# Kernel optimization log

Hardware: AMD Instinct MI355X
Metric: run time of the kernel (lower is better)

## Reference

```python
import jax, jax.numpy as jnp
from jax import lax
import numpy as np
from itertools import permutations, combinations

GRID = (8, 8, 8)  # width, height, depth


def _build_complex(size):
    """Freudenthal (Kuhn) triangulation of the 3D voxel grid.

    Equivalent role to scipy Delaunay on the regular grid (which is degenerate
    anyway): 6 tetrahedra per unit cube, plus all unique faces, edges, verts.
    Returns:
      simp_verts [n,4] int32 : vertex ids of each simplex, padded by repetition
      simp_dim   [n]   int32 : simplex dimension 0..3
      bnd_cof, bnd_face [m] int32 : (cofacet_id, face_id) boundary incidences
    """
    W, H, D = size

    def vid(p):
        return (p[..., 0] * H + p[..., 1]) * D + p[..., 2]

    e = np.eye(3, dtype=np.int64)
    gx, gy, gz = np.meshgrid(np.arange(W - 1), np.arange(H - 1), np.arange(D - 1), indexing="ij")
    base = np.stack([gx, gy, gz], -1).reshape(-1, 3)
    tet_list = []
    for p in permutations(range(3)):
        v0 = base
        v1 = v0 + e[p[0]]
        v2 = v1 + e[p[1]]
        v3 = v2 + e[p[2]]
        tet_list.append(np.stack([vid(v0), vid(v1), vid(v2), vid(v3)], -1))
    tets = np.unique(np.sort(np.concatenate(tet_list, 0), axis=1), axis=0)
    c3 = np.array(list(combinations(range(4), 3)))
    tris = np.unique(tets[:, c3].reshape(-1, 3), axis=0)
    c2 = np.array(list(combinations(range(3), 2)))
    edges = np.unique(tris[:, c2].reshape(-1, 2), axis=0)

    nV = W * H * D
    nE, nT = len(edges), len(tris)
    eid = {tuple(ed): nV + i for i, ed in enumerate(edges)}
    tid = {tuple(tr): nV + nE + i for i, tr in enumerate(tris)}

    bc, bf = [], []
    for i, ed in enumerate(edges):
        j = nV + i
        bc += [j, j]
        bf += [int(ed[0]), int(ed[1])]
    for i, tr in enumerate(tris):
        j = nV + nE + i
        for pair in combinations(tr, 2):
            bc.append(j)
            bf.append(eid[pair])
    for i, te in enumerate(tets):
        j = nV + nE + nT + i
        for tri in combinations(te, 3):
            bc.append(j)
            bf.append(tid[tri])

    vpad = np.repeat(np.arange(nV)[:, None], 4, axis=1)
    epad = np.pad(edges, ((0, 0), (0, 2)), mode="edge")
    tpad = np.pad(tris, ((0, 0), (0, 1)), mode="edge")
    simp_verts = np.concatenate([vpad, epad, tpad, tets], 0).astype(np.int32)
    simp_dim = np.concatenate([
        np.zeros(nV), np.ones(nE), 2 * np.ones(nT), 3 * np.ones(len(tets))
    ]).astype(np.int32)
    return simp_verts, simp_dim, np.asarray(bc, np.int32), np.asarray(bf, np.int32)


def setup_inputs() -> dict:
    key = jax.random.key(0)
    sv, sd, bc, bf = _build_complex(GRID)
    beta = jax.random.normal(key, (GRID[0] * GRID[1] * GRID[2],), dtype=jnp.float32)
    return {
        "beta": beta,
        "simp_verts": jnp.asarray(sv),
        "simp_dim": jnp.asarray(sd),
        "bnd_cof": jnp.asarray(bc),
        "bnd_face": jnp.asarray(bf),
    }


def _toploss(beta, simp_verts, simp_dim, bnd_cof, bnd_face):
    n = simp_dim.shape[0]
    # Superlevel-set (sublevel=False) filtration: simplex value = min over vertices.
    f = jnp.min(beta[simp_verts], axis=1)  # [n]
    # Filtration order: f descending, tie-break dimension ascending.
    perm = jnp.lexsort((simp_dim, lax.stop_gradient(-f)))
    inv = jnp.zeros(n, jnp.int32).at[perm].set(jnp.arange(n, dtype=jnp.int32))
    # Boundary matrix over GF(2), stored row-major: B[j] = boundary of simplex j.
    B = jnp.zeros((n, n), dtype=bool).at[inv[bnd_cof], inv[bnd_face]].set(True)

    idxs = jnp.arange(n, dtype=jnp.int32)
    low = lambda row: jnp.max(jnp.where(row, idxs, -1))

    def body(j, state):
        B, piv = state

        def cond(c):
            return (c[1] >= 0) & (piv[c[1]] >= 0)

        def step(c):
            r = c[0] ^ B[piv[c[1]]]
            return r, low(r)

        row = B[j]
        row, l = lax.while_loop(cond, step, (row, low(row)))
        B = B.at[j].set(row)
        piv2 = piv.at[jnp.maximum(l, 0)].set(jnp.asarray(j, jnp.int32))
        piv = jnp.where(l >= 0, piv2, piv)
        return B, piv

    _, piv = lax.fori_loop(0, n, body, (B, jnp.full((n,), -1, jnp.int32)))
    piv = lax.stop_gradient(piv)  # combinatorial pairing: constant wrt beta

    fs = f[perm]           # filtration values in sorted order (differentiable)
    ds = simp_dim[perm]
    paired = piv >= 0      # simplex i born, killed by simplex piv[i]
    lengths = jnp.where(paired, fs - fs[jnp.maximum(piv, 0)], 0.0)  # birth - death >= 0
    # SumBarcodeLengths(dim=0): all finite dim-0 bars (essential bars have length 0).
    loss0 = jnp.sum(jnp.where(ds == 0, lengths, 0.0))
    # PartialSumBarcodeLengths(dim=1, skip=1): sum of dim-1 lengths minus the largest.
    len1 = jnp.where(ds == 1, lengths, 0.0)
    loss1 = jnp.sum(len1) - jnp.max(len1)
    return loss0 + loss1


_toploss_jit = jax.jit(_toploss)


def reference(beta, simp_verts, simp_dim, bnd_cof, bnd_face):
    return _toploss_jit(beta, simp_verts, simp_dim, bnd_cof, bnd_face)
```

## Files before the change

### kernel.cpp

```cpp
#include <hip/hip_runtime.h>
#include <stdint.h>

#define MAX_E 3072
#define MAX_T 4608
#define MAX_V 1024
#define TW    72
#define INF_I 0x7fffffff
#define RB_E  12
#define RB_T  18
#define RB_C  24
#define TBLK  18
#define EP_BITS  14
#define EP_MASK  0x3FFF
#define EP_DONE  0x3FFF

typedef unsigned long long ull;

__device__ int   g_erank[MAX_E];
__device__ int   g_eorder[MAX_E];
__device__ float g_ef[MAX_E];
__device__ int   g_trank[MAX_T];
__device__ float g_tf[MAX_T];
__device__ __attribute__((aligned(16))) ull g_rows[(size_t)MAX_E * TW];
__device__ int   g_mst[MAX_E];
__device__ int   g_clr[MAX_E];
__device__ int   g_ilow[MAX_E];
__device__ float g_loss0;

__device__ __forceinline__ int ub_dim(const int* __restrict__ sd, int nS, int d) {
  int lo = 0, hi = nS;
  while (lo < hi) { int mid = (lo + hi) >> 1; if (sd[mid] <= d) lo = mid + 1; else hi = mid; }
  return lo;
}

__device__ __forceinline__ ull rank_key(float f, int j) {
  unsigned bb = __float_as_uint(f);
  unsigned ord = (bb & 0x80000000u) ? ~bb : (bb | 0x80000000u);
  return ((ull)ord << 32) | (ull)(0xffffffffu - (unsigned)j);
}

__device__ __forceinline__ int rank_count64(const ull* __restrict__ sk, int n, ull ki) {
  int r = 0, j = 0;
  for (; j + 8 <= n; j += 8) {
    ulonglong2 a = *(const ulonglong2*)(sk + j);
    ulonglong2 b = *(const ulonglong2*)(sk + j + 2);
    ulonglong2 c = *(const ulonglong2*)(sk + j + 4);
    ulonglong2 d = *(const ulonglong2*)(sk + j + 6);
    r += (int)(a.x > ki) + (int)(a.y > ki) + (int)(b.x > ki) + (int)(b.y > ki)
       + (int)(c.x > ki) + (int)(c.y > ki) + (int)(d.x > ki) + (int)(d.y > ki);
  }
  for (; j < n; ++j) r += (int)(sk[j] > ki);
  return r;
}

__device__ __forceinline__ int uf_find(int* par, int x) {
  for (;;) {
    int p = par[x];
    if (p == x) return x;
    int gp = par[p];
    if (p != gp) par[x] = gp;
    x = gp;
  }
}

union SharedK1 {
  struct { alignas(16) ull sk[MAX_T]; } rank;
  struct {
    int par[MAX_V]; ull cand[MAX_V]; int hookTo[MAX_V];
    int eu[MAX_E], ev2[MAX_E];
    float efv[MAX_E];
    unsigned int ekey[MAX_E];
    unsigned short alive[2][MAX_E];
    unsigned char mstf[MAX_E];
  } uf;
};

__global__ void __launch_bounds__(256) k_main1(const float* __restrict__ beta,
                                               const int* __restrict__ sv,
                                               const int* __restrict__ sd,
                                               int nV, int nS) {
  __shared__ SharedK1 sh;
  __shared__ float aS[4], aM[4], aW[4];
  __shared__ int nNext;
  int b = blockIdx.x, tid = threadIdx.x;
  int nE = ub_dim(sd, nS, 1) - nV;

  if (b < RB_E) {
    int i = b * 256 + tid;
    float fi = 0.f;
    for (int j = tid; j < nE; j += 256) {
      const int* p = &sv[(size_t)(nV + j) * 4];
      float fj = fminf(beta[p[0]], beta[p[1]]);
      if (j == i) fi = fj;
      sh.rank.sk[j] = rank_key(fj, j);
    }
    __syncthreads();
    if (i >= nE) return;
    int r = rank_count64(sh.rank.sk, nE, sh.rank.sk[i]);
    g_erank[i] = r;
    g_eorder[r] = i;
    g_ef[r] = fi;
    return;
  }
  if (b < RB_E + RB_T) {
    int nT = ub_dim(sd, nS, 2) - nV - nE;
    int base = nV + nE;
    int i = (b - RB_E) * 256 + tid;
    float fi = 0.f;
    for (int j = tid; j < nT; j += 256) {
      const int* p = &sv[(size_t)(base + j) * 4];
      float fj = fminf(fminf(beta[p[0]], beta[p[1]]), beta[p[2]]);
      if (j == i) fi = fj;
      sh.rank.sk[j] = rank_key(fj, j);
    }
    __syncthreads();
    if (i >= nT) return;
    int r = rank_count64(sh.rank.sk, nT, sh.rank.sk[i]);
    g_trank[i] = r;
    g_tf[r] = fi;
    return;
  }
  if (b > RB_E + RB_T) {
    size_t i = (size_t)(b - RB_E - RB_T - 1) * 256 + tid;
    size_t stride = (size_t)RB_C * 256;
    for (size_t k = i; k < (size_t)MAX_E * TW; k += stride) g_rows[k] = 0ull;
    for (size_t k = i; k < MAX_E; k += stride) g_ilow[k] = -1;
    return;
  }

  int lane = tid & 63, wave = tid >> 6;
  int* par = sh.uf.par;
  for (int v = tid; v < nV; v += 256) par[v] = v;
  for (int e = tid; e < nE; e += 256) {
    int u = sv[(size_t)(nV + e) * 4];
    int v = sv[(size_t)(nV + e) * 4 + 1];
    sh.uf.eu[e] = u; sh.uf.ev2[e] = v;
    float fe = fminf(beta[u], beta[v]);
    sh.uf.efv[e] = fe;
    unsigned int bb = __float_as_uint(fe);
    sh.uf.ekey[e] = (bb & 0x80000000u) ? ~bb : (bb | 0x80000000u);
    sh.uf.alive[0][e] = (unsigned short)e;
    sh.uf.mstf[e] = 0;
  }
  float s = 0.f, m = -3.0e38f;
  for (int v = tid; v < nV; v += 256) { float fv = beta[v]; s += fv; m = fmaxf(m, fv); }
  float W = 0.f;
  int nAlive = nE, cur = 0;
  __syncthreads();
  for (int phase = 0; phase < 20 && nAlive > 0; ++phase) {
    for (int v = tid; v < nV; v += 256) sh.uf.cand[v] = 0ull;
    if (tid == 0) nNext = 0;
    __syncthreads();
    for (int i0 = 0; i0 < nAlive; i0 += 256) {
      int i = i0 + tid;
      int e = -1;
      bool cross = false;
      int ra = 0, rb = 0;
      if (i < nAlive) {
        e = sh.uf.alive[cur][i];
        ra = uf_find(par, sh.uf.eu[e]);
        rb = uf_find(par, sh.uf.ev2[e]);
        cross = (ra != rb);
      }
      ull mb = __ballot(cross);
      int base = 0;
      if (lane == 0 && mb) base = atomicAdd(&nNext, __popcll(mb));
      base = __shfl(base, 0);
      if (cross) {
        int off = __popcll(mb & ((1ull << lane) - 1ull));
        sh.uf.alive[cur ^ 1][base + off] = (unsigned short)e;
        ull key = ((ull)sh.uf.ekey[e] << 32) | (ull)(0xffffffffu - (unsigned)e);
        atomicMax(&sh.uf.cand[ra], key);
        atomicMax(&sh.uf.cand[rb], key);
      }
    }
    __syncthreads();
    for (int v = tid; v < nV; v += 256) {
      int t = -1;
      ull cv = sh.uf.cand[v];
      if (par[v] == v && cv) {
        int e = (int)(0xffffffffu - (unsigned)(cv & 0xffffffffu));
        int ra = uf_find(par, sh.uf.eu[e]);
        int rb = uf_find(par, sh.uf.ev2[e]);
        int other = (ra == v) ? rb : ra;
        if (sh.uf.cand[other] != cv || v < other) t = other;
      }
      sh.uf.hookTo[v] = t;
    }
    __syncthreads();
    for (int v = tid; v < nV; v += 256) {
      int t = sh.uf.hookTo[v];
      if (t >= 0) {
        par[v] = t;
        int e = (int)(0xffffffffu - (unsigned)(sh.uf.cand[v] & 0xffffffffu));
        W += sh.uf.efv[e];
        sh.uf.mstf[e] = 1;
      }
    }
    __syncthreads();
    for (int it = 0; it < 2; ++it) {
      for (int v = tid; v < nV; v += 256) {
        int p = par[v]; int gp = par[p];
        if (p != gp) par[v] = gp;
      }
      __syncthreads();
    }
    nAlive = nNext;
    cur ^= 1;
    __syncthreads();
  }
  __syncthreads();
  for (int e = tid; e < nE; e += 256) g_mst[e] = sh.uf.mstf[e];
  #pragma unroll
  for (int off = 32; off; off >>= 1) {
    s += __shfl_xor(s, off, 64);
    m = fmaxf(m, __shfl_xor(m, off, 64));
    W += __shfl_xor(W, off, 64);
  }
  if (lane == 0) { aS[wave] = s; aM[wave] = m; aW[wave] = W; }
  __syncthreads();
  if (tid == 0) {
    float S = 0.f, M = -3.0e38f, WW = 0.f;
    for (int i = 0; i < 4; ++i) { S += aS[i]; M = fmaxf(M, aM[i]); WW += aW[i]; }
    g_loss0 = S - M - WW;
  }
}

__global__ void __launch_bounds__(256) k_scat(const int* __restrict__ bf,
                                              const int* __restrict__ sd,
                                              int nV, int nS) {
  int nE = ub_dim(sd, nS, 1) - nV;
  int tid = threadIdx.x;
  if (blockIdx.x == TBLK) {
    for (int r = tid; r < nE; r += 256)
      g_clr[nE - 1 - r] = g_mst[g_eorder[r]];
    return;
  }
  int nT = ub_dim(sd, nS, 2) - nV - nE;
  int t = blockIdx.x * 256 + tid;
  if (t >= nT) return;
  int lpos = nT - 1 - g_trank[t];
  size_t base = (size_t)2 * nE + (size_t)3 * t;
  ull bit = 1ull << (lpos & 63);
  int word = lpos >> 6;
  for (int j = 0; j < 3; ++j) {
    int e = bf[base + j] - nV;
    int rr = nE - 1 - g_erank[e];
    atomicOr(&g_rows[(size_t)rr * TW + word], bit);
    atomicMax(&g_ilow[rr], lpos);
  }
}

__device__ __forceinline__ int row_low(ull x, ull y, int lane) {
  ull msk = __ballot((x | y) != 0ull);
  int hb = y ? (lane * 128 + 127 - __clzll(y)) : (lane * 128 + 63 - __clzll(x | 1ull));
  return msk ? __shfl(hb, 63 - __clzll(msk)) : -1;
}

__global__ void __launch_bounds__(1024) k_reduce(const int* __restrict__ sd,
                                                 int nV, int nS,
                                                 float* __restrict__ out) {
  __shared__ int spiv[MAX_T];
  __shared__ int lowA[MAX_E];
  __shared__ int lists[2][MAX_E];
  __shared__ int tailq[64];
  __shared__ int cnts[2];
  __shared__ int workIdx;
  __shared__ float ssum[16], smax[16];

  int tid = threadIdx.x;
  int lane = tid & 63;
  int wave = tid >> 6;
  int nE = ub_dim(sd, nS, 1) - nV;
  int nT = ub_dim(sd, nS, 2) - nV - nE;

  for (int i = tid; i < nT; i += 1024) spiv[i] = INF_I;
  if (tid == 0) { cnts[0] = 0; cnts[1] = 0; }
  __syncthreads();

  for (int r = tid; r < nE; r += 1024) {
    int l = g_clr[r] ? -1 : g_ilow[r];
    lowA[r] = l;
    if (l >= 0) atomicMin(&spiv[l], (r << EP_BITS) | EP_DONE);
  }
  __syncthreads();
  for (int r = tid; r < nE; r += 1024) {
    int l = lowA[r];
    if (l >= 0 && (spiv[l] >> EP_BITS) != r) { int q = atomicAdd(&cnts[0], 1); lists[0][q] = r; }
  }
  __syncthreads();

  int pass = 0;
  int cnt = cnts[0];
  while (cnt > 0 && pass < 16000) {
    int cur = pass & 1, nxt = cur ^ 1;

    if (cnt <= 8) {
      if (wave == 0) {
        for (int i = lane; i < cnt; i += 64) tailq[i] = lists[cur][i];
        int head = 0, tl = cnt;
        while (head < tl) {
          int r = tailq[head & 63]; head++;
          int l = lowA[r];
          ull wx = 0, wy = 0;
          bool loaded = false;
          for (;;) {
            int p = spiv[l] >> EP_BITS;
            ull px = 0, py = 0;
            if (lane < 36) {
              ulonglong2 v = *(const ulonglong2*)&g_rows[(size_t)p * TW + 2 * lane];
              px = v.x; py = v.y;
            }
            if (!loaded) {
              if (lane < 36) {
                ulonglong2 v = *(const ulonglong2*)&g_rows[(size_t)r * TW + 2 * lane];
                wx = v.x; wy = v.y;
              }
              loaded = true;
            }
            wx ^= px; wy ^= py;
            l = row_low(wx, wy, lane);
            if (l < 0) break;
            int old = 0;
            if (lane == 0) old = atomicMin(&spiv[l], (r << EP_BITS) | EP_DONE);
            old = __shfl(old, 0);
            if (old > ((r << EP_BITS) | EP_DONE)) {
              if (lane < 36) {
                ulonglong2 v; v.x = wx; v.y = wy;
                *(ulonglong2*)&g_rows[(size_t)r * TW + 2 * lane] = v;
              }
              if (lane == 0) lowA[r] = l;
              if (old != INF_I) { if (lane == 0) tailq[tl & 63] = old >> EP_BITS; tl++; }
              break;
            }
          }
        }
      }
      __syncthreads();
      break;
    }

    if (tid == 0) { cnts[nxt] = 0; workIdx = 0; }
    __syncthreads();
    for (;;) {
      int idx = 0;
      if (lane == 0) idx = atomicAdd(&workIdx, 1);
      idx = __shfl(idx, 0);
      if (idx >= cnt) break;
      int r = lists[cur][idx];
      int l = lowA[r];
      ull wx = 0, wy = 0;
      bool loaded = false, modified = false;
      for (;;) {
        int val = spiv[l];
        int p = val >> EP_BITS;
        if ((val & EP_MASK) == pass) {
          if (lane == 0) { int q = atomicAdd(&cnts[nxt], 1); lists[nxt][q] = r; }
          break;
        }
        ull px = 0, py = 0;
        if (lane < 36) {
          ulonglong2 v = *(const ulonglong2*)&g_rows[(size_t)p * TW + 2 * lane];
          px = v.x; py = v.y;
        }
        if (!loaded) {
          if (lane < 36) {
            ulonglong2 v = *(const ulonglong2*)&g_rows[(size_t)r * TW + 2 * lane];
            wx = v.x; wy = v.y;
          }
          loaded = true;
        }
        wx ^= px; wy ^= py;
        modified = true;
        l = row_low(wx, wy, lane);
        if (lane == 0) lowA[r] = l;
        if (l < 0) break;
        int myval = (r << EP_BITS) | pass;
        int old = 0;
        if (lane == 0) old = atomicMin(&spiv[l], myval);
        old = __shfl(old, 0);
        if (old > myval) {
          if (old != INF_I && lane == 0) { int q = atomicAdd(&cnts[nxt], 1); lists[nxt][q] = old >> EP_BITS; }
          break;
        }
      }
      if (modified && l >= 0 && lane < 36) {
        ulonglong2 v; v.x = wx; v.y = wy;
        *(ulonglong2*)&g_rows[(size_t)r * TW + 2 * lane] = v;
      }
    }
    __syncthreads();
    cnt = cnts[nxt];
    pass++;
  }

  float sum = 0.f, mx = 0.f;
  for (int l = tid; l < nT; l += 1024) {
    int v = spiv[l];
    if (v != INF_I) {
      int r = v >> EP_BITS;
      float len = g_ef[nE - 1 - r] - g_tf[nT - 1 - l];
      sum += len;
      mx = fmaxf(mx, len);
    }
  }
  #pragma unroll
  for (int off = 32; off; off >>= 1) {
    sum += __shfl_xor(sum, off, 64);
    mx = fmaxf(mx, __shfl_xor(mx, off, 64));
  }
  if (lane == 0) { ssum[wave] = sum; smax[wave] = mx; }
  __syncthreads();
  if (tid == 0) {
    float S = 0.f, M = 0.f;
    for (int i = 0; i < 16; ++i) { S += ssum[i]; M = fmaxf(M, smax[i]); }
    out[0] = g_loss0 + S - M;
  }
}

extern "C" void kernel_launch(void* const* d_in, const int* in_sizes, int n_in,
                              void* d_out, int out_size, void* d_ws, size_t ws_size,
                              hipStream_t stream) {
  const float* beta = (const float*)d_in[0];
  const int*   sv   = (const int*)d_in[1];
  const int*   sd   = (const int*)d_in[2];
  const int*   bf   = (const int*)d_in[4];
  float* out = (float*)d_out;

  int nV = in_sizes[0];
  int nS = in_sizes[2];

  k_main1<<<RB_E + RB_T + 1 + RB_C, 256, 0, stream>>>(beta, sv, sd, nV, nS);
  k_scat<<<TBLK + 1, 256, 0, stream>>>(bf, sd, nV, nS);
  k_reduce<<<1, 1024, 0, stream>>>(sd, nV, nS, out);
}
```

Measured before the change: 172.6 us.

## Rotate row buffers so pivot rows stay readable during concurrent reduction

Replaces the single global row matrix with four rotating copies. Each row is written to a fresh buffer slot before its pivot claim is published, and that slot index is encoded in the low bits of the pivot word. Readers can then use a pivot row that another wave is still updating, which removes the per-pass epoch check that deferred such rows to the next pass. In exchange every reduction step writes the whole row to global memory and adds a block-level fence, and correctness relies on three rotating slots being enough to avoid overwriting a row that is still being read.

```diff
diff --git a/kernel.cpp b/kernel.cpp
--- a/kernel.cpp
+++ b/kernel.cpp
@@ -10,9 +10,6 @@
 #define RB_T  18
 #define RB_C  24
 #define TBLK  18
-#define EP_BITS  14
-#define EP_MASK  0x3FFF
-#define EP_DONE  0x3FFF
 
 typedef unsigned long long ull;
 
@@ -21,7 +18,7 @@
 __device__ float g_ef[MAX_E];
 __device__ int   g_trank[MAX_T];
 __device__ float g_tf[MAX_T];
-__device__ __attribute__((aligned(16))) ull g_rows[(size_t)MAX_E * TW];
+__device__ __attribute__((aligned(16))) ull g_rowsA[4][(size_t)MAX_E * TW];
 __device__ int   g_mst[MAX_E];
 __device__ int   g_clr[MAX_E];
 __device__ int   g_ilow[MAX_E];
@@ -123,7 +120,7 @@
   if (b > RB_E + RB_T) {
     size_t i = (size_t)(b - RB_E - RB_T - 1) * 256 + tid;
     size_t stride = (size_t)RB_C * 256;
-    for (size_t k = i; k < (size_t)MAX_E * TW; k += stride) g_rows[k] = 0ull;
+    for (size_t k = i; k < (size_t)MAX_E * TW; k += stride) g_rowsA[0][k] = 0ull;
     for (size_t k = i; k < MAX_E; k += stride) g_ilow[k] = -1;
     return;
   }
@@ -246,7 +243,7 @@
   for (int j = 0; j < 3; ++j) {
     int e = bf[base + j] - nV;
     int rr = nE - 1 - g_erank[e];
-    atomicOr(&g_rows[(size_t)rr * TW + word], bit);
+    atomicOr(&g_rowsA[0][(size_t)rr * TW + word], bit);
     atomicMax(&g_ilow[rr], lpos);
   }
 }
@@ -262,6 +259,7 @@
                                                  float* __restrict__ out) {
   __shared__ int spiv[MAX_T];
   __shared__ int lowA[MAX_E];
+  __shared__ unsigned char rot[MAX_E];
   __shared__ int lists[2][MAX_E];
   __shared__ int tailq[64];
   __shared__ int cnts[2];
@@ -275,18 +273,19 @@
   int nT = ub_dim(sd, nS, 2) - nV - nE;
 
   for (int i = tid; i < nT; i += 1024) spiv[i] = INF_I;
+  for (int r = tid; r < nE; r += 1024) rot[r] = 0;
   if (tid == 0) { cnts[0] = 0; cnts[1] = 0; }
   __syncthreads();
 
   for (int r = tid; r < nE; r += 1024) {
     int l = g_clr[r] ? -1 : g_ilow[r];
     lowA[r] = l;
-    if (l >= 0) atomicMin(&spiv[l], (r << EP_BITS) | EP_DONE);
+    if (l >= 0) atomicMin(&spiv[l], r << 2);
   }
   __syncthreads();
   for (int r = tid; r < nE; r += 1024) {
     int l = lowA[r];
-    if (l >= 0 && (spiv[l] >> EP_BITS) != r) { int q = atomicAdd(&cnts[0], 1); lists[0][q] = r; }
+    if (l >= 0 && (spiv[l] >> 2) != r) { int q = atomicAdd(&cnts[0], 1); lists[0][q] = r; }
   }
   __syncthreads();
 
@@ -302,38 +301,42 @@
         while (head < tl) {
           int r = tailq[head & 63]; head++;
           int l = lowA[r];
+          int rt = rot[r];
+          int sb = (rt == 0) ? 0 : 1 + ((rt - 1) % 3);
           ull wx = 0, wy = 0;
-          bool loaded = false;
+          if (lane < 36) {
+            ulonglong2 v = *(const ulonglong2*)&g_rowsA[sb][(size_t)r * TW + 2 * lane];
+            wx = v.x; wy = v.y;
+          }
+          int val = spiv[l];
           for (;;) {
-            int p = spiv[l] >> EP_BITS;
+            int p = val >> 2, pb = val & 3;
             ull px = 0, py = 0;
             if (lane < 36) {
-              ulonglong2 v = *(const ulonglong2*)&g_rows[(size_t)p * TW + 2 * lane];
+              ulonglong2 v = *(const ulonglong2*)&g_rowsA[pb][(size_t)p * TW + 2 * lane];
               px = v.x; py = v.y;
-            }
-            if (!loaded) {
-              if (lane < 36) {
-                ulonglong2 v = *(const ulonglong2*)&g_rows[(size_t)r * TW + 2 * lane];
-                wx = v.x; wy = v.y;
-              }
-              loaded = true;
             }
             wx ^= px; wy ^= py;
             l = row_low(wx, wy, lane);
             if (l < 0) break;
+            int nb = 1 + (rt % 3); rt++;
+            if (lane < 36) {
+              ulonglong2 v; v.x = wx; v.y = wy;
+              *(ulonglong2*)&g_rowsA[nb][(size_t)r * TW + 2 * lane] = v;
+            }
+            __threadfence_block();
+            int myval = (r << 2) | nb;
             int old = 0;
-            if (lane == 0) old = atomicMin(&spiv[l], (r << EP_BITS) | EP_DONE);
+            if (lane == 0) old = atomicMin(&spiv[l], myval);
             old = __shfl(old, 0);
-            if (old > ((r << EP_BITS) | EP_DONE)) {
-              if (lane < 36) {
-                ulonglong2 v; v.x = wx; v.y = wy;
-                *(ulonglong2*)&g_rows[(size_t)r * TW + 2 * lane] = v;
-              }
-              if (lane == 0) lowA[r] = l;
-              if (old != INF_I) { if (lane == 0) tailq[tl & 63] = old >> EP_BITS; tl++; }
+            if (old > myval) {
+              if (lane == 0) { lowA[r] = l; rot[r] = (unsigned char)rt; }
+              if (old != INF_I) { if (lane == 0) tailq[tl & 63] = old >> 2; tl++; }
               break;
             }
+            val = old;
           }
+          if (l < 0 && lane == 0) rot[r] = (unsigned char)rt;
         }
       }
       __syncthreads();
@@ -349,45 +352,45 @@
       if (idx >= cnt) break;
       int r = lists[cur][idx];
       int l = lowA[r];
+      int rt = rot[r];
+      int sb = (rt == 0) ? 0 : 1 + ((rt - 1) % 3);
       ull wx = 0, wy = 0;
-      bool loaded = false, modified = false;
+      if (lane < 36) {
+        ulonglong2 v = *(const ulonglong2*)&g_rowsA[sb][(size_t)r * TW + 2 * lane];
+        wx = v.x; wy = v.y;
+      }
+      int val = spiv[l];
       for (;;) {
-        int val = spiv[l];
-        int p = val >> EP_BITS;
-        if ((val & EP_MASK) == pass) {
-          if (lane == 0) { int q = atomicAdd(&cnts[nxt], 1); lists[nxt][q] = r; }
-          break;
-        }
+        int p = val >> 2, pb = val & 3;
         ull px = 0, py = 0;
         if (lane < 36) {
-          ulonglong2 v = *(const ulonglong2*)&g_rows[(size_t)p * TW + 2 * lane];
+          ulonglong2 v = *(const ulonglong2*)&g_rowsA[pb][(size_t)p * TW + 2 * lane];
           px = v.x; py = v.y;
         }
-        if (!loaded) {
-          if (lane < 36) {
-            ulonglong2 v = *(const ulonglong2*)&g_rows[(size_t)r * TW + 2 * lane];
-            wx = v.x; wy = v.y;
-          }
-          loaded = true;
-        }
         wx ^= px; wy ^= py;
-        modified = true;
         l = row_low(wx, wy, lane);
         if (lane == 0) lowA[r] = l;
         if (l < 0) break;
-        int myval = (r << EP_BITS) | pass;
+        int nb = 1 + (rt % 3); rt++;
+        if (lane < 36) {
+          ulonglong2 v; v.x = wx; v.y = wy;
+          *(ulonglong2*)&g_rowsA[nb][(size_t)r * TW + 2 * lane] = v;
+        }
+        __threadfence_block();
+        int myval = (r << 2) | nb;
         int old = 0;
         if (lane == 0) old = atomicMin(&spiv[l], myval);
         old = __shfl(old, 0);
         if (old > myval) {
-          if (old != INF_I && lane == 0) { int q = atomicAdd(&cnts[nxt], 1); lists[nxt][q] = old >> EP_BITS; }
+          if (lane == 0) {
+            rot[r] = (unsigned char)rt;
+            if (old != INF_I) { int q = atomicAdd(&cnts[nxt], 1); lists[nxt][q] = old >> 2; }
+          }
           break;
         }
-      }
-      if (modified && l >= 0 && lane < 36) {
-        ulonglong2 v; v.x = wx; v.y = wy;
-        *(ulonglong2*)&g_rows[(size_t)r * TW + 2 * lane] = v;
-      }
+        val = old;
+      }
+      if (l < 0 && lane == 0) rot[r] = (unsigned char)rt;
     }
     __syncthreads();
     cnt = cnts[nxt];
@@ -398,7 +401,7 @@
   for (int l = tid; l < nT; l += 1024) {
     int v = spiv[l];
     if (v != INF_I) {
-      int r = v >> EP_BITS;
+      int r = v >> 2;
       float len = g_ef[nE - 1 - r] - g_tf[nT - 1 - l];
       sum += len;
       mx = fmaxf(mx, len);
```

Measured after the change: 188.6 us. 9.3% more time.

## Fuse scatter and reduction kernels with a global completion counter

Applied to the files above, without the earlier changes.

Merges the boundary-matrix scatter kernel and the single-block column reduction kernel into one launch. Blocks 1..SCAT_B do the scatter and block SCAT_B+1 does the clearing permutation. Each of these signals completion through an atomic counter, and block 0 spin-waits on that counter before it starts reducing. This removes one kernel launch and its boundary gap. The cost is a spin-wait that assumes all blocks are co-resident, and the counter is reset by k_main1.

```diff
diff --git a/kernel.cpp b/kernel.cpp
--- a/kernel.cpp
+++ b/kernel.cpp
@@ -9,7 +9,7 @@
 #define RB_E  12
 #define RB_T  18
 #define RB_C  24
-#define TBLK  18
+#define SCAT_B 5
 #define EP_BITS  14
 #define EP_MASK  0x3FFF
 #define EP_DONE  0x3FFF
@@ -25,6 +25,7 @@
 __device__ int   g_mst[MAX_E];
 __device__ int   g_clr[MAX_E];
 __device__ int   g_ilow[MAX_E];
+__device__ int   g_done;
 __device__ float g_loss0;
 
 __device__ __forceinline__ int ub_dim(const int* __restrict__ sd, int nS, int d) {
@@ -129,6 +130,7 @@
   }
 
   int lane = tid & 63, wave = tid >> 6;
+  if (tid == 0) g_done = 0;
   int* par = sh.uf.par;
   for (int v = tid; v < nV; v += 256) par[v] = v;
   for (int e = tid; e < nE; e += 256) {
@@ -226,40 +228,48 @@
   }
 }
 
-__global__ void __launch_bounds__(256) k_scat(const int* __restrict__ bf,
-                                              const int* __restrict__ sd,
-                                              int nV, int nS) {
-  int nE = ub_dim(sd, nS, 1) - nV;
-  int tid = threadIdx.x;
-  if (blockIdx.x == TBLK) {
-    for (int r = tid; r < nE; r += 256)
-      g_clr[nE - 1 - r] = g_mst[g_eorder[r]];
-    return;
-  }
-  int nT = ub_dim(sd, nS, 2) - nV - nE;
-  int t = blockIdx.x * 256 + tid;
-  if (t >= nT) return;
-  int lpos = nT - 1 - g_trank[t];
-  size_t base = (size_t)2 * nE + (size_t)3 * t;
-  ull bit = 1ull << (lpos & 63);
-  int word = lpos >> 6;
-  for (int j = 0; j < 3; ++j) {
-    int e = bf[base + j] - nV;
-    int rr = nE - 1 - g_erank[e];
-    atomicOr(&g_rows[(size_t)rr * TW + word], bit);
-    atomicMax(&g_ilow[rr], lpos);
-  }
-}
-
 __device__ __forceinline__ int row_low(ull x, ull y, int lane) {
   ull msk = __ballot((x | y) != 0ull);
   int hb = y ? (lane * 128 + 127 - __clzll(y)) : (lane * 128 + 63 - __clzll(x | 1ull));
   return msk ? __shfl(hb, 63 - __clzll(msk)) : -1;
 }
 
-__global__ void __launch_bounds__(1024) k_reduce(const int* __restrict__ sd,
-                                                 int nV, int nS,
-                                                 float* __restrict__ out) {
+__global__ void __launch_bounds__(1024) k_scatred(const int* __restrict__ bf,
+                                                  const int* __restrict__ sd,
+                                                  int nV, int nS,
+                                                  float* __restrict__ out) {
+  int tid = threadIdx.x;
+  int nE = ub_dim(sd, nS, 1) - nV;
+  int nT = ub_dim(sd, nS, 2) - nV - nE;
+
+  if (blockIdx.x >= 1 && blockIdx.x <= SCAT_B) {
+    int t = (blockIdx.x - 1) * 1024 + tid;
+    if (t < nT) {
+      int lpos = nT - 1 - g_trank[t];
+      size_t base = (size_t)2 * nE + (size_t)3 * t;
+      ull bit = 1ull << (lpos & 63);
+      int word = lpos >> 6;
+      for (int j = 0; j < 3; ++j) {
+        int e = bf[base + j] - nV;
+        int rr = nE - 1 - g_erank[e];
+        atomicOr(&g_rows[(size_t)rr * TW + word], bit);
+        atomicMax(&g_ilow[rr], lpos);
+      }
+    }
+    __syncthreads();
+    __threadfence();
+    if (tid == 0) atomicAdd(&g_done, 1);
+    return;
+  }
+  if (blockIdx.x == SCAT_B + 1) {
+    for (int r = tid; r < nE; r += 1024)
+      g_clr[nE - 1 - r] = g_mst[g_eorder[r]];
+    __syncthreads();
+    __threadfence();
+    if (tid == 0) atomicAdd(&g_done, 1);
+    return;
+  }
+
   __shared__ int spiv[MAX_T];
   __shared__ int lowA[MAX_E];
   __shared__ int lists[2][MAX_E];
@@ -268,15 +278,15 @@
   __shared__ int workIdx;
   __shared__ float ssum[16], smax[16];
 
-  int tid = threadIdx.x;
   int lane = tid & 63;
   int wave = tid >> 6;
-  int nE = ub_dim(sd, nS, 1) - nV;
-  int nT = ub_dim(sd, nS, 2) - nV - nE;
 
   for (int i = tid; i < nT; i += 1024) spiv[i] = INF_I;
   if (tid == 0) { cnts[0] = 0; cnts[1] = 0; }
   __syncthreads();
+  if (tid == 0) { while (atomicAdd(&g_done, 0) < SCAT_B + 1) { } }
+  __syncthreads();
+  __threadfence();
 
   for (int r = tid; r < nE; r += 1024) {
     int l = g_clr[r] ? -1 : g_ilow[r];
@@ -431,6 +441,5 @@
   int nS = in_sizes[2];
 
   k_main1<<<RB_E + RB_T + 1 + RB_C, 256, 0, stream>>>(beta, sv, sd, nV, nS);
-  k_scat<<<TBLK + 1, 256, 0, stream>>>(bf, sd, nV, nS);
-  k_reduce<<<1, 1024, 0, stream>>>(sd, nV, nS, out);
-}
+  k_scatred<<<SCAT_B + 2, 1024, 0, stream>>>(bf, sd, nV, nS, out);
+}
```

Result: slower. 182.9 us (+6.0%).

## Chase displaced pivots in-warp instead of deferring them to next pass

Applied to the files above, without the earlier changes.

Restructures the lock-free parallel column reduction. A warp now first tries to claim the pivot slot with atomicMin. When it wins and displaces an older-epoch owner, it writes back its row and immediately continues reducing the displaced row, rather than appending that row to the next pass's work list. This is meant to cut the number of passes and block-wide barriers in the phased reduction. The cost is more complex control flow and extra row stores on every successful claim.

```diff
diff --git a/kernel.cpp b/kernel.cpp
--- a/kernel.cpp
+++ b/kernel.cpp
@@ -351,42 +351,75 @@
       int l = lowA[r];
       ull wx = 0, wy = 0;
       bool loaded = false, modified = false;
+      bool do_claim = true;
+      int val = 0;
       for (;;) {
-        int val = spiv[l];
-        int p = val >> EP_BITS;
-        if ((val & EP_MASK) == pass) {
-          if (lane == 0) { int q = atomicAdd(&cnts[nxt], 1); lists[nxt][q] = r; }
-          break;
+        if (do_claim) {
+          int myval = (r << EP_BITS) | pass;
+          int old = 0;
+          if (lane == 0) old = atomicMin(&spiv[l], myval);
+          old = __shfl(old, 0);
+          if (old > myval) {
+            if (!loaded) {
+              if (lane < 36) {
+                ulonglong2 v = *(const ulonglong2*)&g_rows[(size_t)r * TW + 2 * lane];
+                wx = v.x; wy = v.y;
+              }
+              loaded = true;
+            }
+            if (lane < 36) {
+              ulonglong2 v; v.x = wx; v.y = wy;
+              *(ulonglong2*)&g_rows[(size_t)r * TW + 2 * lane] = v;
+            }
+            if (lane == 0) lowA[r] = l;
+            if (old == INF_I) break;
+            int op = old >> EP_BITS;
+            int oep = old & EP_MASK;
+            if (oep == pass) {
+              if (lane == 0) { int q = atomicAdd(&cnts[nxt], 1); lists[nxt][q] = op; }
+              break;
+            }
+            ull qx = 0, qy = 0;
+            if (lane < 36) {
+              ulonglong2 v = *(const ulonglong2*)&g_rows[(size_t)op * TW + 2 * lane];
+              qx = v.x; qy = v.y;
+            }
+            wx ^= qx; wy ^= qy;
+            r = op; modified = true; loaded = true;
+            l = row_low(wx, wy, lane);
+            if (l < 0) break;
+          } else {
+            val = old;
+            do_claim = false;
+          }
+        } else {
+          int p = val >> EP_BITS;
+          if ((val & EP_MASK) == pass) {
+            if (modified && lane < 36) {
+              ulonglong2 v; v.x = wx; v.y = wy;
+              *(ulonglong2*)&g_rows[(size_t)r * TW + 2 * lane] = v;
+            }
+            if (lane == 0) { lowA[r] = l; int q = atomicAdd(&cnts[nxt], 1); lists[nxt][q] = r; }
+            break;
+          }
+          ull px = 0, py = 0;
+          if (lane < 36) {
+            ulonglong2 v = *(const ulonglong2*)&g_rows[(size_t)p * TW + 2 * lane];
+            px = v.x; py = v.y;
+          }
+          if (!loaded) {
+            if (lane < 36) {
+              ulonglong2 v = *(const ulonglong2*)&g_rows[(size_t)r * TW + 2 * lane];
+              wx = v.x; wy = v.y;
+            }
+            loaded = true;
+          }
+          wx ^= px; wy ^= py;
+          modified = true;
+          l = row_low(wx, wy, lane);
+          if (l < 0) break;
+          do_claim = true;
         }
-        ull px = 0, py = 0;
-        if (lane < 36) {
-          ulonglong2 v = *(const ulonglong2*)&g_rows[(size_t)p * TW + 2 * lane];
-          px = v.x; py = v.y;
-        }
-        if (!loaded) {
-          if (lane < 36) {
-            ulonglong2 v = *(const ulonglong2*)&g_rows[(size_t)r * TW + 2 * lane];
-            wx = v.x; wy = v.y;
-          }
-          loaded = true;
-        }
-        wx ^= px; wy ^= py;
-        modified = true;
-        l = row_low(wx, wy, lane);
-        if (lane == 0) lowA[r] = l;
-        if (l < 0) break;
-        int myval = (r << EP_BITS) | pass;
-        int old = 0;
-        if (lane == 0) old = atomicMin(&spiv[l], myval);
-        old = __shfl(old, 0);
-        if (old > myval) {
-          if (old != INF_I && lane == 0) { int q = atomicAdd(&cnts[nxt], 1); lists[nxt][q] = old >> EP_BITS; }
-          break;
-        }
-      }
-      if (modified && l >= 0 && lane < 36) {
-        ulonglong2 v; v.x = wx; v.y = wy;
-        *(ulonglong2*)&g_rows[(size_t)r * TW + 2 * lane] = v;
       }
     }
     __syncthreads();
```

New measurement: 170.9 us. About the same (-1.0%).
